# Performance work log

Hardware: AMD Instinct MI355X
Metric: run time of the kernel (lower is better)

Reference implementation:

```python
import jax, jax.numpy as jnp
import numpy as np
from jax import lax

SIGMAS = (15.0, 80.0, 250.0)
DETAIL_WEIGHT = 0.0
ILLUM_WEIGHT = 1.0
EPS = 0.001


def _gaussian_kernel1d(sigma: float) -> np.ndarray:
    ks = int(2 * round(3 * sigma) + 1)
    if ks % 2 == 0:
        ks += 1
    x = np.arange(ks, dtype=np.float32) - (ks - 1) / 2.0
    k = np.exp(-0.5 * (x / sigma) ** 2)
    return (k / k.sum()).astype(np.float32)


def _gaussian_blur(img: jnp.ndarray, sigma: float) -> jnp.ndarray:
    # Separable Gaussian blur with reflect padding (kornia gaussian_blur2d semantics).
    k = jnp.asarray(_gaussian_kernel1d(sigma))
    ks = k.shape[0]
    p = ks // 2
    C = img.shape[1]
    dn = ('NCHW', 'OIHW', 'NCHW')
    kv = jnp.broadcast_to(k.reshape(1, 1, ks, 1), (C, 1, ks, 1))  # vertical pass
    kh = jnp.broadcast_to(k.reshape(1, 1, 1, ks), (C, 1, 1, ks))  # horizontal pass
    x = jnp.pad(img, ((0, 0), (0, 0), (p, p), (0, 0)), mode='reflect')
    x = lax.conv_general_dilated(x, kv, (1, 1), 'VALID', dimension_numbers=dn,
                                 feature_group_count=C)
    x = jnp.pad(x, ((0, 0), (0, 0), (0, 0), (p, p)), mode='reflect')
    x = lax.conv_general_dilated(x, kh, (1, 1), 'VALID', dimension_numbers=dn,
                                 feature_group_count=C)
    return x


def _multi_scale_retinex(input_img: jnp.ndarray) -> jnp.ndarray:
    img = jnp.clip(input_img, EPS, 1.0)
    log_img = jnp.log(img)
    acc = jnp.zeros_like(log_img)
    for sigma in SIGMAS:
        blur = jnp.maximum(_gaussian_blur(img, sigma), EPS)
        acc = acc + (log_img - jnp.log(blur))
    return acc / len(SIGMAS)


def setup_inputs() -> dict:
    key = jax.random.key(0)
    input_img = jax.random.uniform(key, (2, 3, 1024, 1024), dtype=jnp.float32)
    return {"input_img": input_img}


def reference(input_img):
    reflectance = _multi_scale_retinex(input_img)
    gx = reflectance[:, :, :, :-1] - reflectance[:, :, :, 1:]
    gy = reflectance[:, :, :-1, :] - reflectance[:, :, 1:, :]
    loss_detail = jnp.abs(gx).mean() + jnp.abs(gy).mean()
    illumination = jnp.log(jnp.maximum(input_img, EPS)) - reflectance
    igx = illumination[:, :, :, :-1] - illumination[:, :, :, 1:]
    igy = illumination[:, :, :-1, :] - illumination[:, :, 1:, :]
    loss_smooth_illum = jnp.abs(igx).mean() + jnp.abs(igy).mean()
    loss = DETAIL_WEIGHT * loss_detail + ILLUM_WEIGHT * loss_smooth_illum
    return (loss, loss_detail, loss_smooth_illum, reflectance, illumination)
```

## Files before the change

### kernel.cpp

```cpp
#include <hip/hip_runtime.h>
#include <math.h>

#define IMN 1024
#define IMGSZ (IMN * IMN)
#define NIMG 6
#define EPSV 0.001f
#define NB1 4096

typedef unsigned short u16;
typedef _Float16 f16;
typedef __attribute__((ext_vector_type(8))) _Float16 half8;
typedef __attribute__((ext_vector_type(16))) float floatx16;

__device__ __forceinline__ u16 f16_bits(float v) {
  union { f16 h; u16 b; } u;
  u.h = (f16)v;
  return u.b;
}
__device__ __forceinline__ float f16_val(u16 b) {
  union { f16 h; u16 b2; } u;
  u.b2 = b;
  return (float)u.h;
}
__device__ __forceinline__ void unp4(uint2 v, float* o) {
  o[0] = f16_val((u16)(v.x & 0xffff));
  o[1] = f16_val((u16)(v.x >> 16));
  o[2] = f16_val((u16)(v.y & 0xffff));
  o[3] = f16_val((u16)(v.y >> 16));
}

__global__ __launch_bounds__(256) void prep_k(const float* __restrict__ inp,
                                              u16* __restrict__ H,
                                              u16* __restrict__ LI,
                                              u16* __restrict__ WF) {
  int y = blockIdx.y;
  int tid = threadIdx.x;
  if (y == 3) {
#pragma unroll
    for (int r2 = 0; r2 < 6; r2++) {
      int i4 = ((r2 * 1024 + blockIdx.x) << 10) + tid * 4;
      float4 v = *(const float4*)&inp[i4];
      float x[4] = {v.x, v.y, v.z, v.w};
      u16 h[4], l[4];
#pragma unroll
      for (int e = 0; e < 4; e++) {
        h[e] = f16_bits(fminf(fmaxf(x[e], EPSV), 1.f));
        l[e] = f16_bits(logf(fmaxf(x[e], EPSV)));
      }
      *(uint2*)&H[i4] = make_uint2((unsigned)h[0] | ((unsigned)h[1] << 16),
                                   (unsigned)h[2] | ((unsigned)h[3] << 16));
      *(uint2*)&LI[i4] = make_uint2((unsigned)l[0] | ((unsigned)l[1] << 16),
                                    (unsigned)l[2] | ((unsigned)l[3] << 16));
    }
    return;
  }
  const int kss[3] = {91, 481, 1501};
  const float sg[3] = {15.f, 80.f, 250.f};
  int ks = kss[y];
  float sigma = sg[y];
  int r = blockIdx.x;
  int p = ks >> 1;
  float ctr = (float)(ks - 1) * 0.5f;
  __shared__ float red[256];
  __shared__ float row[IMN];
  float loc = 0.f;
  for (int t = tid; t < ks; t += 256) {
    float x = ((float)t - ctr) / sigma;
    loc += expf(-0.5f * x * x);
  }
  red[tid] = loc;
  __syncthreads();
  for (int o = 128; o > 0; o >>= 1) {
    if (tid < o) red[tid] += red[tid + o];
    __syncthreads();
  }
  float inv = 1.f / red[0];
  for (int i2 = tid; i2 < IMN; i2 += 256) row[i2] = 0.f;
  __syncthreads();
  for (int t = tid; t < ks; t += 256) {
    float x = ((float)t - ctr) / sigma;
    float v = expf(-0.5f * x * x) * inv;
    int q = r + t - p;
    int j = q < 0 ? -q : (q > IMN - 1 ? 2 * (IMN - 1) - q : q);
    atomicAdd(&row[j], v);
  }
  __syncthreads();
  for (int i2 = tid; i2 < IMN; i2 += 256)
    WF[(size_t)y * IMGSZ + (size_t)r * IMN + i2] = f16_bits(row[i2] * 256.f);
}

template <int EPI>
__global__ __launch_bounds__(256, 4) void gemm_pass(
    const u16* __restrict__ AH, const u16* __restrict__ WF,
    u16* __restrict__ OH, u16* __restrict__ LB16, int sBase, int outByZ, int rmw) {
  __shared__ u16 smem[2 * 128 * 32 + 256];
  u16* Af = smem;
  u16* Bf = smem + 128 * 32;
  int z = blockIdx.z;
  int zs = z / 6;
  int s = (gridDim.z >= 18) ? (sBase + 2 - zs) : (sBase + zs);
  int i = z - zs * 6;
  const u16* Ag = AH + (size_t)(EPI == 0 ? i : z) * IMGSZ;
  const u16* Bg = WF + (size_t)s * IMGSZ;
  int bm = blockIdx.y * 128, bn = blockIdx.x * 128;
  int tid = threadIdx.x;
  int lane = tid & 63, w = tid >> 6;
  int wm = (w >> 1) * 64, wn = (w & 1) * 64;
  int lrow = lane & 31, lh = lane >> 5;
  int sig = (lrow >> 1) & 3;
  int tr = tid >> 2;
  int tc = (tid & 3) * 8;
  int sslot = ((tid & 3) ^ ((tr >> 1) & 3)) * 8;
  floatx16 acc[2][2] = {};

  int p = (s == 0) ? 45 : (s == 1) ? 240 : 750;
  int klo = bn - p;
  klo = (klo < 0 ? 0 : klo) & ~31;
  int khi = bn + 128 + p;
  if (khi > IMN) khi = IMN;

  for (int k0 = klo; k0 < khi; k0 += 32) {
    uint4 a0 = *(const uint4*)&Ag[(size_t)(bm + tr) * IMN + k0 + tc];
    uint4 a1 = *(const uint4*)&Ag[(size_t)(bm + tr + 64) * IMN + k0 + tc];
    uint4 b0 = *(const uint4*)&Bg[(size_t)(bn + tr) * IMN + k0 + tc];
    uint4 b1 = *(const uint4*)&Bg[(size_t)(bn + tr + 64) * IMN + k0 + tc];
    *(uint4*)&Af[tr * 32 + sslot] = a0;
    *(uint4*)&Af[(tr + 64) * 32 + sslot] = a1;
    *(uint4*)&Bf[tr * 32 + sslot] = b0;
    *(uint4*)&Bf[(tr + 64) * 32 + sslot] = b1;
    __syncthreads();
#pragma unroll
    for (int kk = 0; kk < 32; kk += 16) {
      int sl = (kk >> 3) + lh;
      int so = ((sl ^ sig) * 8);
      half8 ah[2], bh[2];
#pragma unroll
      for (int mt = 0; mt < 2; mt++)
        ah[mt] = *(const half8*)&Af[(wm + mt * 32 + lrow) * 32 + so];
#pragma unroll
      for (int nt2 = 0; nt2 < 2; nt2++)
        bh[nt2] = *(const half8*)&Bf[(wn + nt2 * 32 + lrow) * 32 + so];
#pragma unroll
      for (int mt = 0; mt < 2; mt++)
#pragma unroll
        for (int nt2 = 0; nt2 < 2; nt2++)
          acc[mt][nt2] = __builtin_amdgcn_mfma_f32_32x32x16_f16(ah[mt], bh[nt2], acc[mt][nt2], 0, 0, 0);
    }
    __syncthreads();
  }

  float* lf = (float*)smem + w * 1056;
#pragma unroll
  for (int mt = 0; mt < 2; mt++)
#pragma unroll
    for (int nt = 0; nt < 2; nt++) {
#pragma unroll
      for (int rq = 0; rq < 4; rq++)
#pragma unroll
        for (int e = 0; e < 4; e++)
          lf[lrow * 33 + rq * 8 + lh * 4 + e] = acc[mt][nt][rq * 4 + e];
      __syncthreads();
#pragma unroll
      for (int p4 = 0; p4 < 4; p4++) {
        int rl = p4 * 8 + (lane >> 3);
        int cl = (lane & 7) * 4;
        float v0 = lf[rl * 33 + cl + 0];
        float v1 = lf[rl * 33 + cl + 1];
        float v2 = lf[rl * 33 + cl + 2];
        float v3 = lf[rl * 33 + cl + 3];
        int gn = bn + wn + nt * 32 + rl;
        int gm = bm + wm + mt * 32 + cl;
        if (EPI == 0) {
          size_t go = (size_t)z * IMGSZ + (size_t)gn * IMN + gm;
          *(uint2*)&OH[go] = make_uint2(
              (unsigned)f16_bits(v0) | ((unsigned)f16_bits(v1) << 16),
              (unsigned)f16_bits(v2) | ((unsigned)f16_bits(v3) << 16));
        } else {
          const float us = 0x1p-16f;
          size_t go = (size_t)(outByZ ? z : i) * IMGSZ + (size_t)gn * IMN + gm;
          float r0 = logf(fmaxf(v0 * us, EPSV));
          float r1 = logf(fmaxf(v1 * us, EPSV));
          float r2 = logf(fmaxf(v2 * us, EPSV));
          float r3 = logf(fmaxf(v3 * us, EPSV));
          if (rmw) {
            uint2 pa = *(const uint2*)&LB16[go];
            float o4[4];
            unp4(pa, o4);
            r0 += o4[0]; r1 += o4[1]; r2 += o4[2]; r3 += o4[3];
          }
          *(uint2*)&LB16[go] = make_uint2(
              (unsigned)f16_bits(r0) | ((unsigned)f16_bits(r1) << 16),
              (unsigned)f16_bits(r2) | ((unsigned)f16_bits(r3) << 16));
        }
      }
      __syncthreads();
    }
}

__global__ __launch_bounds__(256) void loss_stage1_k(const u16* __restrict__ li,
                                                     const u16* __restrict__ lb, int three,
                                                     float* __restrict__ refl,
                                                     float* __restrict__ illum,
                                                     float* __restrict__ pd,
                                                     float* __restrict__ ps) {
  const int S = NIMG * IMGSZ;
  const int NCH = S >> 2;
  const int stride = NB1 * 256;
  const float third = 1.f / 3.f;
  float sd = 0.f, ss = 0.f;
  for (int c = blockIdx.x * 256 + threadIdx.x; c < NCH; c += stride) {
    int i = c << 2;
    int col = i & (IMN - 1);
    int row = (i >> 10) & (IMN - 1);
    bool hR = col < (IMN - 4);
    bool hD = row < (IMN - 1);
    float sum[5];
    {
      float t0[4];
      unp4(*(const uint2*)&lb[i], t0);
      sum[0] = t0[0]; sum[1] = t0[1]; sum[2] = t0[2]; sum[3] = t0[3];
      sum[4] = hR ? f16_val(lb[i + 4]) : 0.f;
      if (three) {
        float t1[4], t2[4];
        unp4(*(const uint2*)&lb[i + S], t1);
        unp4(*(const uint2*)&lb[i + 2 * S], t2);
#pragma unroll
        for (int j = 0; j < 4; j++) sum[j] += t1[j] + t2[j];
        if (hR) sum[4] += f16_val(lb[i + 4 + S]) + f16_val(lb[i + 4 + 2 * S]);
      }
    }
    float Iv[5], Rv[5], LIv[4];
#pragma unroll
    for (int j = 0; j < 5; j++) Iv[j] = sum[j] * third;
    unp4(*(const uint2*)&li[i], LIv);
#pragma unroll
    for (int j = 0; j < 4; j++) Rv[j] = LIv[j] - Iv[j];
    if (hR) Rv[4] = f16_val(li[i + 4]) - Iv[4];
#pragma unroll
    for (int j = 0; j < 4; j++) {
      refl[i + j] = Rv[j];
      illum[i + j] = Iv[j];
    }
#pragma unroll
    for (int j = 0; j < 3; j++) {
      sd += fabsf(Rv[j] - Rv[j + 1]);
      ss += fabsf(Iv[j] - Iv[j + 1]);
    }
    if (hR) {
      sd += fabsf(Rv[3] - Rv[4]);
      ss += fabsf(Iv[3] - Iv[4]);
    }
    if (hD) {
      int ib = i + IMN;
      float sb[4];
      {
        float t0[4];
        unp4(*(const uint2*)&lb[ib], t0);
        sb[0] = t0[0]; sb[1] = t0[1]; sb[2] = t0[2]; sb[3] = t0[3];
        if (three) {
          float t1[4], t2[4];
          unp4(*(const uint2*)&lb[ib + S], t1);
          unp4(*(const uint2*)&lb[ib + 2 * S], t2);
#pragma unroll
          for (int j = 0; j < 4; j++) sb[j] += t1[j] + t2[j];
        }
      }
      float LBv[4];
      unp4(*(const uint2*)&li[ib], LBv);
#pragma unroll
      for (int j = 0; j < 4; j++) {
        float Ib = sb[j] * third;
        float Rb = LBv[j] - Ib;
        sd += fabsf(Rv[j] - Rb);
        ss += fabsf(Iv[j] - Ib);
      }
    }
  }
  for (int o = 32; o > 0; o >>= 1) {
    sd += __shfl_down(sd, o);
    ss += __shfl_down(ss, o);
  }
  __shared__ float rsd[4], rss[4];
  int lane = threadIdx.x & 63, w = threadIdx.x >> 6;
  if (lane == 0) { rsd[w] = sd; rss[w] = ss; }
  __syncthreads();
  if (threadIdx.x == 0) {
    pd[blockIdx.x] = rsd[0] + rsd[1] + rsd[2] + rsd[3];
    ps[blockIdx.x] = rss[0] + rss[1] + rss[2] + rss[3];
  }
}

__global__ __launch_bounds__(256) void loss_stage2_k(const float* __restrict__ pd,
                                                     const float* __restrict__ ps,
                                                     float* __restrict__ out) {
  float sd = 0.f, ss = 0.f;
  for (int i = threadIdx.x; i < NB1; i += 256) {
    sd += pd[i];
    ss += ps[i];
  }
  for (int o = 32; o > 0; o >>= 1) {
    sd += __shfl_down(sd, o);
    ss += __shfl_down(ss, o);
  }
  __shared__ float rsd[4], rss[4];
  int lane = threadIdx.x & 63, w = threadIdx.x >> 6;
  if (lane == 0) { rsd[w] = sd; rss[w] = ss; }
  __syncthreads();
  if (threadIdx.x == 0) {
    float tsd = rsd[0] + rsd[1] + rsd[2] + rsd[3];
    float tss = rss[0] + rss[1] + rss[2] + rss[3];
    const float sc = 1.f / 6285312.f;
    out[0] = tss * sc;
    out[1] = tsd * sc;
    out[2] = tss * sc;
  }
}

extern "C" void kernel_launch(void* const* d_in, const int* in_sizes, int n_in,
                              void* d_out, int out_size, void* d_ws, size_t ws_size,
                              hipStream_t stream) {
  const float* inp = (const float*)d_in[0];
  float* out = (float*)d_out;
  float* refl = out + 3;
  float* illum = refl + (size_t)NIMG * IMGSZ;

  char* p = (char*)d_ws;
  float* pd = (float*)p;
  float* ps = pd + NB1;
  p += 32768;
  u16* WF = (u16*)p;                        p += (size_t)3 * IMGSZ * 2;
  u16* imgF = (u16*)p;                      p += (size_t)NIMG * IMGSZ * 2;
  u16* logI = (u16*)p;                      p += (size_t)NIMG * IMGSZ * 2;
  size_t fixed = (size_t)(p - (char*)d_ws);
  size_t needT1 = fixed + (size_t)18 * IMGSZ * 2 + (size_t)18 * IMGSZ * 2;
  bool t1 = ws_size >= needT1;
  int nz = t1 ? 18 : 6;
  u16* UtH = (u16*)p;                       p += (size_t)nz * IMGSZ * 2;
  u16* LB = (u16*)p;

  prep_k<<<dim3(1024, 4), 256, 0, stream>>>(inp, imgF, logI, WF);

  if (t1) {
    dim3 g(8, 8, 18);
    gemm_pass<0><<<g, 256, 0, stream>>>(imgF, WF, UtH, nullptr, 0, 1, 0);
    gemm_pass<1><<<g, 256, 0, stream>>>(UtH, WF, nullptr, LB, 0, 1, 0);
  } else {
    dim3 g(8, 8, 6);
    for (int s = 0; s < 3; s++) {
      gemm_pass<0><<<g, 256, 0, stream>>>(imgF, WF, UtH, nullptr, s, 0, 0);
      gemm_pass<1><<<g, 256, 0, stream>>>(UtH, WF, nullptr, LB, s, 0, s > 0);
    }
  }
  loss_stage1_k<<<NB1, 256, 0, stream>>>(logI, LB, t1 ? 1 : 0, refl, illum, pd, ps);
  loss_stage2_k<<<1, 256, 0, stream>>>(pd, ps, out);
}
```

Before: 223.9 us.

## Process two image planes per GEMM block to share Gaussian weight tiles

Each GEMM block now computes two image planes against the same weight tile, loading the B tile into shared memory once and issuing MFMAs for both A tiles. The grid z dimension is halved and launch bounds drop to 2 blocks per CU to fit the doubled accumulators. This cuts B-tile global loads and LDS traffic per output. In exchange it raises register pressure, lowers occupancy and leaves fewer blocks in flight, which may hurt latency hiding.

```diff
diff --git a/kernel.cpp b/kernel.cpp
--- a/kernel.cpp
+++ b/kernel.cpp
@@ -90,17 +90,22 @@
 }
 
 template <int EPI>
-__global__ __launch_bounds__(256, 4) void gemm_pass(
+__global__ __launch_bounds__(256, 2) void gemm_pair(
     const u16* __restrict__ AH, const u16* __restrict__ WF,
     u16* __restrict__ OH, u16* __restrict__ LB16, int sBase, int outByZ, int rmw) {
-  __shared__ u16 smem[2 * 128 * 32 + 256];
-  u16* Af = smem;
-  u16* Bf = smem + 128 * 32;
+  __shared__ u16 smem[3 * 128 * 32];
+  u16* A0 = smem;
+  u16* A1 = smem + 4096;
+  u16* Bf = smem + 8192;
   int z = blockIdx.z;
-  int zs = z / 6;
-  int s = (gridDim.z >= 18) ? (sBase + 2 - zs) : (sBase + zs);
-  int i = z - zs * 6;
-  const u16* Ag = AH + (size_t)(EPI == 0 ? i : z) * IMGSZ;
+  int s = (gridDim.z >= 9) ? (2 - z / 3) : sBase;
+  int pr = z - (z / 3) * 3;
+  int i0 = 2 * pr, i1 = i0 + 1;
+  int zp0 = (2 - s) * 6 + i0;
+  int up0 = outByZ ? zp0 : i0;
+  int up1 = up0 + 1;
+  const u16* Ag0 = AH + (size_t)(EPI == 0 ? i0 : up0) * IMGSZ;
+  const u16* Ag1 = AH + (size_t)(EPI == 0 ? i1 : up1) * IMGSZ;
   const u16* Bg = WF + (size_t)s * IMGSZ;
   int bm = blockIdx.y * 128, bn = blockIdx.x * 128;
   int tid = threadIdx.x;
@@ -111,7 +116,8 @@
   int tr = tid >> 2;
   int tc = (tid & 3) * 8;
   int sslot = ((tid & 3) ^ ((tr >> 1) & 3)) * 8;
-  floatx16 acc[2][2] = {};
+  floatx16 acc0[2][2] = {};
+  floatx16 acc1[2][2] = {};
 
   int p = (s == 0) ? 45 : (s == 1) ? 240 : 750;
   int klo = bn - p;
@@ -120,12 +126,16 @@
   if (khi > IMN) khi = IMN;
 
   for (int k0 = klo; k0 < khi; k0 += 32) {
-    uint4 a0 = *(const uint4*)&Ag[(size_t)(bm + tr) * IMN + k0 + tc];
-    uint4 a1 = *(const uint4*)&Ag[(size_t)(bm + tr + 64) * IMN + k0 + tc];
+    uint4 a00 = *(const uint4*)&Ag0[(size_t)(bm + tr) * IMN + k0 + tc];
+    uint4 a01 = *(const uint4*)&Ag0[(size_t)(bm + tr + 64) * IMN + k0 + tc];
+    uint4 a10 = *(const uint4*)&Ag1[(size_t)(bm + tr) * IMN + k0 + tc];
+    uint4 a11 = *(const uint4*)&Ag1[(size_t)(bm + tr + 64) * IMN + k0 + tc];
     uint4 b0 = *(const uint4*)&Bg[(size_t)(bn + tr) * IMN + k0 + tc];
     uint4 b1 = *(const uint4*)&Bg[(size_t)(bn + tr + 64) * IMN + k0 + tc];
-    *(uint4*)&Af[tr * 32 + sslot] = a0;
-    *(uint4*)&Af[(tr + 64) * 32 + sslot] = a1;
+    *(uint4*)&A0[tr * 32 + sslot] = a00;
+    *(uint4*)&A0[(tr + 64) * 32 + sslot] = a01;
+    *(uint4*)&A1[tr * 32 + sslot] = a10;
+    *(uint4*)&A1[(tr + 64) * 32 + sslot] = a11;
     *(uint4*)&Bf[tr * 32 + sslot] = b0;
     *(uint4*)&Bf[(tr + 64) * 32 + sslot] = b1;
     __syncthreads();
@@ -133,68 +143,78 @@
     for (int kk = 0; kk < 32; kk += 16) {
       int sl = (kk >> 3) + lh;
       int so = ((sl ^ sig) * 8);
-      half8 ah[2], bh[2];
-#pragma unroll
-      for (int mt = 0; mt < 2; mt++)
-        ah[mt] = *(const half8*)&Af[(wm + mt * 32 + lrow) * 32 + so];
+      half8 ah0[2], ah1[2], bh[2];
+#pragma unroll
+      for (int mt = 0; mt < 2; mt++) {
+        int ro = (wm + mt * 32 + lrow) * 32 + so;
+        ah0[mt] = *(const half8*)&A0[ro];
+        ah1[mt] = *(const half8*)&A1[ro];
+      }
 #pragma unroll
       for (int nt2 = 0; nt2 < 2; nt2++)
         bh[nt2] = *(const half8*)&Bf[(wn + nt2 * 32 + lrow) * 32 + so];
 #pragma unroll
       for (int mt = 0; mt < 2; mt++)
 #pragma unroll
-        for (int nt2 = 0; nt2 < 2; nt2++)
-          acc[mt][nt2] = __builtin_amdgcn_mfma_f32_32x32x16_f16(ah[mt], bh[nt2], acc[mt][nt2], 0, 0, 0);
+        for (int nt2 = 0; nt2 < 2; nt2++) {
+          acc0[mt][nt2] = __builtin_amdgcn_mfma_f32_32x32x16_f16(ah0[mt], bh[nt2], acc0[mt][nt2], 0, 0, 0);
+          acc1[mt][nt2] = __builtin_amdgcn_mfma_f32_32x32x16_f16(ah1[mt], bh[nt2], acc1[mt][nt2], 0, 0, 0);
+        }
     }
     __syncthreads();
   }
 
   float* lf = (float*)smem + w * 1056;
 #pragma unroll
-  for (int mt = 0; mt < 2; mt++)
-#pragma unroll
-    for (int nt = 0; nt < 2; nt++) {
-#pragma unroll
-      for (int rq = 0; rq < 4; rq++)
-#pragma unroll
-        for (int e = 0; e < 4; e++)
-          lf[lrow * 33 + rq * 8 + lh * 4 + e] = acc[mt][nt][rq * 4 + e];
-      __syncthreads();
-#pragma unroll
-      for (int p4 = 0; p4 < 4; p4++) {
-        int rl = p4 * 8 + (lane >> 3);
-        int cl = (lane & 7) * 4;
-        float v0 = lf[rl * 33 + cl + 0];
-        float v1 = lf[rl * 33 + cl + 1];
-        float v2 = lf[rl * 33 + cl + 2];
-        float v3 = lf[rl * 33 + cl + 3];
-        int gn = bn + wn + nt * 32 + rl;
-        int gm = bm + wm + mt * 32 + cl;
-        if (EPI == 0) {
-          size_t go = (size_t)z * IMGSZ + (size_t)gn * IMN + gm;
-          *(uint2*)&OH[go] = make_uint2(
-              (unsigned)f16_bits(v0) | ((unsigned)f16_bits(v1) << 16),
-              (unsigned)f16_bits(v2) | ((unsigned)f16_bits(v3) << 16));
-        } else {
-          const float us = 0x1p-16f;
-          size_t go = (size_t)(outByZ ? z : i) * IMGSZ + (size_t)gn * IMN + gm;
-          float r0 = logf(fmaxf(v0 * us, EPSV));
-          float r1 = logf(fmaxf(v1 * us, EPSV));
-          float r2 = logf(fmaxf(v2 * us, EPSV));
-          float r3 = logf(fmaxf(v3 * us, EPSV));
-          if (rmw) {
-            uint2 pa = *(const uint2*)&LB16[go];
-            float o4[4];
-            unp4(pa, o4);
-            r0 += o4[0]; r1 += o4[1]; r2 += o4[2]; r3 += o4[3];
+  for (int im = 0; im < 2; im++) {
+    size_t uplane = (size_t)(im == 0 ? up0 : up1);
+#pragma unroll
+    for (int mt = 0; mt < 2; mt++)
+#pragma unroll
+      for (int nt = 0; nt < 2; nt++) {
+#pragma unroll
+        for (int rq = 0; rq < 4; rq++)
+#pragma unroll
+          for (int e = 0; e < 4; e++)
+            lf[lrow * 33 + rq * 8 + lh * 4 + e] =
+                (im == 0 ? acc0[mt][nt][rq * 4 + e] : acc1[mt][nt][rq * 4 + e]);
+        __syncthreads();
+#pragma unroll
+        for (int p4 = 0; p4 < 4; p4++) {
+          int rl = p4 * 8 + (lane >> 3);
+          int cl = (lane & 7) * 4;
+          float v0 = lf[rl * 33 + cl + 0];
+          float v1 = lf[rl * 33 + cl + 1];
+          float v2 = lf[rl * 33 + cl + 2];
+          float v3 = lf[rl * 33 + cl + 3];
+          int gn = bn + wn + nt * 32 + rl;
+          int gm = bm + wm + mt * 32 + cl;
+          if (EPI == 0) {
+            size_t go = uplane * IMGSZ + (size_t)gn * IMN + gm;
+            *(uint2*)&OH[go] = make_uint2(
+                (unsigned)f16_bits(v0) | ((unsigned)f16_bits(v1) << 16),
+                (unsigned)f16_bits(v2) | ((unsigned)f16_bits(v3) << 16));
+          } else {
+            const float us = 0x1p-16f;
+            size_t go = uplane * IMGSZ + (size_t)gn * IMN + gm;
+            float r0 = logf(fmaxf(v0 * us, EPSV));
+            float r1 = logf(fmaxf(v1 * us, EPSV));
+            float r2 = logf(fmaxf(v2 * us, EPSV));
+            float r3 = logf(fmaxf(v3 * us, EPSV));
+            if (rmw) {
+              uint2 pa = *(const uint2*)&LB16[go];
+              float o4[4];
+              unp4(pa, o4);
+              r0 += o4[0]; r1 += o4[1]; r2 += o4[2]; r3 += o4[3];
+            }
+            *(uint2*)&LB16[go] = make_uint2(
+                (unsigned)f16_bits(r0) | ((unsigned)f16_bits(r1) << 16),
+                (unsigned)f16_bits(r2) | ((unsigned)f16_bits(r3) << 16));
           }
-          *(uint2*)&LB16[go] = make_uint2(
-              (unsigned)f16_bits(r0) | ((unsigned)f16_bits(r1) << 16),
-              (unsigned)f16_bits(r2) | ((unsigned)f16_bits(r3) << 16));
         }
-      }
-      __syncthreads();
-    }
+        __syncthreads();
+      }
+  }
 }
 
 __global__ __launch_bounds__(256) void loss_stage1_k(const u16* __restrict__ li,
@@ -341,14 +361,14 @@
   prep_k<<<dim3(1024, 4), 256, 0, stream>>>(inp, imgF, logI, WF);
 
   if (t1) {
-    dim3 g(8, 8, 18);
-    gemm_pass<0><<<g, 256, 0, stream>>>(imgF, WF, UtH, nullptr, 0, 1, 0);
-    gemm_pass<1><<<g, 256, 0, stream>>>(UtH, WF, nullptr, LB, 0, 1, 0);
+    dim3 g(8, 8, 9);
+    gemm_pair<0><<<g, 256, 0, stream>>>(imgF, WF, UtH, nullptr, 0, 1, 0);
+    gemm_pair<1><<<g, 256, 0, stream>>>(UtH, WF, nullptr, LB, 0, 1, 0);
   } else {
-    dim3 g(8, 8, 6);
+    dim3 g(8, 8, 3);
     for (int s = 0; s < 3; s++) {
-      gemm_pass<0><<<g, 256, 0, stream>>>(imgF, WF, UtH, nullptr, s, 0, 0);
-      gemm_pass<1><<<g, 256, 0, stream>>>(UtH, WF, nullptr, LB, s, 0, s > 0);
+      gemm_pair<0><<<g, 256, 0, stream>>>(imgF, WF, UtH, nullptr, s, 0, 0);
+      gemm_pair<1><<<g, 256, 0, stream>>>(UtH, WF, nullptr, LB, s, 0, s > 0);
     }
   }
   loss_stage1_k<<<NB1, 256, 0, stream>>>(logI, LB, t1 ? 1 : 0, refl, illum, pd, ps);
```

After: 216.8 us. -3.2%, faster.
